# Kernel optimization log

Measured on AMD Instinct MI355X. Metric: run time of the kernel, lower is better.

Reference implementation:

```python
import jax, jax.numpy as jnp
import numpy as np

B, S, H = 1, 1024, 2048
NH, HD = 16, 128
E, K, FI, SFI = 8, 2, 1408, 2816
EPS = 1e-6
THETA = 10000.0


def setup_inputs() -> dict:
    key = jax.random.key(0)
    ks = jax.random.split(key, 14)
    sc = 0.02
    return {
        "hidden_states": jax.random.normal(ks[0], (B, S, H), jnp.float32),
        "ln1_w": jnp.ones((H,), jnp.float32),
        "ln2_w": jnp.ones((H,), jnp.float32),
        "wq": jax.random.normal(ks[1], (H, H), jnp.float32) * sc,
        "wk": jax.random.normal(ks[2], (H, H), jnp.float32) * sc,
        "wv": jax.random.normal(ks[3], (H, H), jnp.float32) * sc,
        "wo": jax.random.normal(ks[4], (H, H), jnp.float32) * sc,
        "gate_w": jax.random.normal(ks[5], (E, H), jnp.float32) * sc,
        "expert_gate": jax.random.normal(ks[6], (E, FI, H), jnp.float32) * sc,
        "expert_up": jax.random.normal(ks[7], (E, FI, H), jnp.float32) * sc,
        "expert_down": jax.random.normal(ks[8], (E, H, FI), jnp.float32) * sc,
        "shared_gate": jax.random.normal(ks[9], (SFI, H), jnp.float32) * sc,
        "shared_up": jax.random.normal(ks[10], (SFI, H), jnp.float32) * sc,
        "shared_down": jax.random.normal(ks[11], (H, SFI), jnp.float32) * sc,
    }


def _rmsnorm(x, w):
    v = jnp.mean(x * x, axis=-1, keepdims=True)
    return x * jax.lax.rsqrt(v + EPS) * w


def _rotate_half(x):
    x1, x2 = x[..., : HD // 2], x[..., HD // 2 :]
    return jnp.concatenate((-x2, x1), axis=-1)


def _rope_cos_sin():
    inv_freq = 1.0 / (THETA ** (jnp.arange(0, HD, 2, dtype=jnp.float32) / HD))
    t = jnp.arange(S, dtype=jnp.float32)
    freqs = t[:, None] * inv_freq[None, :]          # [S, HD//2]
    emb = jnp.concatenate((freqs, freqs), axis=-1)  # [S, HD]
    return jnp.cos(emb)[None, None], jnp.sin(emb)[None, None]  # [1,1,S,HD]


def _decoder_layer(hidden_states, ln1_w, ln2_w, wq, wk, wv, wo, gate_w,
                   expert_gate, expert_up, expert_down,
                   shared_gate, shared_up, shared_down):
    # ---- self-attention ----
    residual = hidden_states
    h = _rmsnorm(hidden_states, ln1_w)
    q = (h @ wq.T).reshape(B, S, NH, HD).transpose(0, 2, 1, 3)  # [B,NH,S,HD]
    k = (h @ wk.T).reshape(B, S, NH, HD).transpose(0, 2, 1, 3)
    v = (h @ wv.T).reshape(B, S, NH, HD).transpose(0, 2, 1, 3)
    cos, sin = _rope_cos_sin()
    q = q * cos + _rotate_half(q) * sin
    k = k * cos + _rotate_half(k) * sin
    scores = jnp.einsum('bhqd,bhkd->bhqk', q, k) / jnp.sqrt(jnp.float32(HD))
    causal = jnp.tril(jnp.ones((S, S), bool))
    scores = jnp.where(causal[None, None], scores, jnp.finfo(jnp.float32).min)
    probs = jax.nn.softmax(scores, axis=-1)
    attn = jnp.einsum('bhqk,bhkd->bhqd', probs, v)
    attn = attn.transpose(0, 2, 1, 3).reshape(B, S, H)
    x = residual + attn @ wo.T

    # ---- MoE MLP ----
    residual = x
    h2 = _rmsnorm(x, ln2_w)
    flat = h2.reshape(-1, H)                       # [N,H], N=B*S
    n_tok = flat.shape[0]
    logits = flat @ gate_w.T                       # [N,E]
    gate_scores = jax.nn.softmax(logits, axis=-1)
    topk_w, topk_idx = jax.lax.top_k(gate_scores, K)
    topk_w = topk_w / (jnp.sum(topk_w, axis=-1, keepdims=True) + 1e-20)
    # dense combine weights [N,E] (zero for unrouted experts)
    combine = jnp.zeros((n_tok, E), flat.dtype).at[
        jnp.arange(n_tok)[:, None], topk_idx].add(topk_w)
    # SwiGLU per expert, dense over all experts, then weighted combine
    g = jnp.einsum('nh,efh->enf', flat, expert_gate)   # [E,N,FI]
    u = jnp.einsum('nh,efh->enf', flat, expert_up)
    act = jax.nn.silu(g) * u
    eo = jnp.einsum('enf,ehf->enh', act, expert_down)  # [E,N,H]
    routed = jnp.einsum('enh,ne->nh', eo, combine)
    # shared experts (always on)
    shared = (jax.nn.silu(flat @ shared_gate.T) * (flat @ shared_up.T)) @ shared_down.T
    return residual + (routed + shared).reshape(B, S, H)


def reference(hidden_states, ln1_w, ln2_w, wq, wk, wv, wo, gate_w,
              expert_gate, expert_up, expert_down,
              shared_gate, shared_up, shared_down):
    return _decoder_layer(hidden_states, ln1_w, ln2_w, wq, wk, wv, wo, gate_w,
                          expert_gate, expert_up, expert_down,
                          shared_gate, shared_up, shared_down)
```

## Files before the change

kernel.cpp:

```cpp
#include <hip/hip_runtime.h>
#include <hip/hip_bf16.h>


#define DI __device__ __forceinline__

typedef __attribute__((ext_vector_type(8))) short short8;
typedef __attribute__((ext_vector_type(4))) float f32x4;
using u16 = unsigned short;

struct alignas(8) U16x4 { u16 x, y, z, w; };

DI u16 f2bf(float f) {
  unsigned u = __float_as_uint(f);
  u += 0x7fffu + ((u >> 16) & 1u);
  return (u16)(u >> 16);
}
DI float bf2f(u16 h) { return __uint_as_float(((unsigned)h) << 16); }

DI void gload16(const void* g, void* l) {
  __builtin_amdgcn_global_load_lds((const __attribute__((address_space(1))) void*)g,
                                   (__attribute__((address_space(3))) void*)l, 16, 0, 0);
}


__global__ __launch_bounds__(256) void k_ropetab(float* __restrict__ tab) {
  int idx = blockIdx.x * 256 + threadIdx.x;
  int s = idx >> 6, i = idx & 63;
  double inv = pow(10000.0, -(double)(2 * i) / 128.0);
  double ang = (double)s * inv;
  tab[idx * 2 + 0] = (float)cos(ang);
  tab[idx * 2 + 1] = (float)sin(ang);
}

__global__ __launch_bounds__(256) void k_rmsnorm(const float* __restrict__ in,
                                                 const float* __restrict__ w,
                                                 float* __restrict__ outf,
                                                 u16* __restrict__ outh,
                                                 u16* __restrict__ outl) {
  const int row = blockIdx.x, t = threadIdx.x;
  const float* x = in + (size_t)row * 2048;
  float4 a = *(const float4*)&x[t * 4];
  float4 b = *(const float4*)&x[1024 + t * 4];
  float ss = a.x * a.x + a.y * a.y + a.z * a.z + a.w * a.w +
             b.x * b.x + b.y * b.y + b.z * b.z + b.w * b.w;
#pragma unroll
  for (int off = 32; off; off >>= 1) ss += __shfl_xor(ss, off);
  __shared__ float red[4];
  if ((t & 63) == 0) red[t >> 6] = ss;
  __syncthreads();
  float total = red[0] + red[1] + red[2] + red[3];
  float r = 1.0f / sqrtf(total * (1.0f / 2048.0f) + 1e-6f);
  float4 wa = *(const float4*)&w[t * 4];
  float4 wb = *(const float4*)&w[1024 + t * 4];
  float va[8] = {a.x * r * wa.x, a.y * r * wa.y, a.z * r * wa.z, a.w * r * wa.w,
                 b.x * r * wb.x, b.y * r * wb.y, b.z * r * wb.z, b.w * r * wb.w};
  if (outf) {
    *(float4*)&outf[(size_t)row * 2048 + t * 4] = make_float4(va[0], va[1], va[2], va[3]);
    *(float4*)&outf[(size_t)row * 2048 + 1024 + t * 4] = make_float4(va[4], va[5], va[6], va[7]);
  }
  if (outh) {
    U16x4 ha{f2bf(va[0]), f2bf(va[1]), f2bf(va[2]), f2bf(va[3])};
    U16x4 hb{f2bf(va[4]), f2bf(va[5]), f2bf(va[6]), f2bf(va[7])};
    *(U16x4*)&outh[(size_t)row * 2048 + t * 4] = ha;
    *(U16x4*)&outh[(size_t)row * 2048 + 1024 + t * 4] = hb;
    if (outl) {
      U16x4 la{f2bf(va[0] - bf2f(ha.x)), f2bf(va[1] - bf2f(ha.y)),
               f2bf(va[2] - bf2f(ha.z)), f2bf(va[3] - bf2f(ha.w))};
      U16x4 lb{f2bf(va[4] - bf2f(hb.x)), f2bf(va[5] - bf2f(hb.y)),
               f2bf(va[6] - bf2f(hb.z)), f2bf(va[7] - bf2f(hb.w))};
      *(U16x4*)&outl[(size_t)row * 2048 + t * 4] = la;
      *(U16x4*)&outl[(size_t)row * 2048 + 1024 + t * 4] = lb;
    }
  }
}

__global__ __launch_bounds__(256) void k_splitf(const float* __restrict__ src,
                                                u16* __restrict__ dh,
                                                u16* __restrict__ dl) {
  int idx = (blockIdx.x * 256 + threadIdx.x) * 4;
  float4 v = *(const float4*)&src[idx];
  U16x4 h{f2bf(v.x), f2bf(v.y), f2bf(v.z), f2bf(v.w)};
  U16x4 l{f2bf(v.x - bf2f(h.x)), f2bf(v.y - bf2f(h.y)),
          f2bf(v.z - bf2f(h.z)), f2bf(v.w - bf2f(h.w))};
  *(U16x4*)&dh[idx] = h;
  *(U16x4*)&dl[idx] = l;
}

__global__ __launch_bounds__(256) void k_rope(float* __restrict__ q, float* __restrict__ k,
                                              const float* __restrict__ tab) {
  int idx = blockIdx.x * 256 + threadIdx.x;
  int s = idx >> 10, rem = idx & 1023;
  int h = rem >> 6, i = rem & 63;
  size_t base = (size_t)s * 2048 + h * 128 + i;
  float c = tab[(s * 64 + i) * 2 + 0];
  float sn = tab[(s * 64 + i) * 2 + 1];
  const float qs = 0.08838834764831845f;
  float q1 = q[base], q2 = q[base + 64];
  q[base] = (q1 * c - q2 * sn) * qs;
  q[base + 64] = (q2 * c + q1 * sn) * qs;
  float k1 = k[base], k2 = k[base + 64];
  k[base] = k1 * c - k2 * sn;
  k[base + 64] = k2 * c + k1 * sn;
}

__global__ __launch_bounds__(256) void k_splitkv(
    const float* __restrict__ qf, const float* __restrict__ kf,
    const float* __restrict__ vf,
    u16* __restrict__ Qh, u16* __restrict__ Ql,
    u16* __restrict__ Kh, u16* __restrict__ Kl,
    u16* __restrict__ Vth, u16* __restrict__ Vtl) {
  int idx = (blockIdx.x * 256 + threadIdx.x) * 4;
  int s = idx >> 11, c = idx & 2047;
  float4 q4 = *(const float4*)&qf[idx];
  U16x4 qh{f2bf(q4.x), f2bf(q4.y), f2bf(q4.z), f2bf(q4.w)};
  U16x4 ql{f2bf(q4.x - bf2f(qh.x)), f2bf(q4.y - bf2f(qh.y)),
           f2bf(q4.z - bf2f(qh.z)), f2bf(q4.w - bf2f(qh.w))};
  *(U16x4*)&Qh[idx] = qh; *(U16x4*)&Ql[idx] = ql;
  float4 k4 = *(const float4*)&kf[idx];
  U16x4 kh{f2bf(k4.x), f2bf(k4.y), f2bf(k4.z), f2bf(k4.w)};
  U16x4 kl{f2bf(k4.x - bf2f(kh.x)), f2bf(k4.y - bf2f(kh.y)),
           f2bf(k4.z - bf2f(kh.z)), f2bf(k4.w - bf2f(kh.w))};
  *(U16x4*)&Kh[idx] = kh; *(U16x4*)&Kl[idx] = kl;
  float4 v4 = *(const float4*)&vf[idx];
  float vv[4] = {v4.x, v4.y, v4.z, v4.w};
#pragma unroll
  for (int i = 0; i < 4; ++i) {
    u16 hv = f2bf(vv[i]);
    u16 lv = f2bf(vv[i] - bf2f(hv));
    Vth[(size_t)(c + i) * 1024 + s] = hv;
    Vtl[(size_t)(c + i) * 1024 + s] = lv;
  }
}

DI void stage_kv(const u16* __restrict__ Khg, const u16* __restrict__ Klg,
                 const u16* __restrict__ Vhg, const u16* __restrict__ Vlg,
                 u16* lsKh, u16* lsKl, u16* lsVh, u16* lsVl,
                 int kvb, int hh, int wv, int lane) {
#pragma unroll
  for (int it = 0; it < 4; ++it) {
    const int ebase = it * 2048 + wv * 512;
    const int eo = ebase + lane * 8;
    {
      const int rr = eo >> 7, cg = (eo >> 3) & 15;
      const size_t src = (size_t)(kvb + rr) * 2048 + hh * 128 + ((cg ^ (rr & 7)) << 3);
      gload16(Khg + src, lsKh + ebase);
      gload16(Klg + src, lsKl + ebase);
    }
    {
      const int rr = eo >> 6, cg = (eo >> 3) & 7;
      const size_t src = (size_t)(hh * 128 + rr) * 1024 + kvb + ((cg ^ (rr & 7)) << 3);
      gload16(Vhg + src, lsVh + ebase);
      gload16(Vlg + src, lsVl + ebase);
    }
  }
}

__global__ __launch_bounds__(256) void k_attn_tile(
    const u16* __restrict__ Qh, const u16* __restrict__ Ql,
    const u16* __restrict__ Khg, const u16* __restrict__ Klg,
    const u16* __restrict__ Vhg, const u16* __restrict__ Vlg,
    u16* __restrict__ atth, u16* __restrict__ attl) {
  __shared__ u16 lsKh[2][8192], lsKl[2][8192], lsVh[2][8192], lsVl[2][8192];
  __shared__ u16 Plh[4][16][72], Pll[4][16][72];
  const int hh = blockIdx.y;
  const int qb = blockIdx.x * 64;
  const int tid = threadIdx.x, lane = tid & 63, wv = tid >> 6;
  const int l15 = lane & 15, grp = lane >> 4;
  u16(*plh)[72] = Plh[wv];
  u16(*pll)[72] = Pll[wv];
  const int q_glob = qb + wv * 16 + l15;
  const int tend = blockIdx.x + 1;

  short8 qfh[4], qfl[4];
  const size_t qbase = (size_t)q_glob * 2048 + hh * 128;
#pragma unroll
  for (int c = 0; c < 4; ++c) {
    qfh[c] = *(const short8*)&Qh[qbase + c * 32 + grp * 8];
    qfl[c] = *(const short8*)&Ql[qbase + c * 32 + grp * 8];
  }
  f32x4 oacc[8];
#pragma unroll
  for (int dc = 0; dc < 8; ++dc) oacc[dc] = 0.f;
  float m_run = -1e30f, l_run = 0.f;

  int cur = 0;
  stage_kv(Khg, Klg, Vhg, Vlg, lsKh[0], lsKl[0], lsVh[0], lsVl[0], 0, hh, wv, lane);
  __syncthreads();

  for (int kt = 0; kt < tend; ++kt) {
    const int kvb = kt * 64;
    if (kt + 1 < tend)
      stage_kv(Khg, Klg, Vhg, Vlg, lsKh[cur ^ 1], lsKl[cur ^ 1], lsVh[cur ^ 1],
               lsVl[cur ^ 1], kvb + 64, hh, wv, lane);
    const u16* kh = lsKh[cur];
    const u16* kl = lsKl[cur];
    const u16* vh = lsVh[cur];
    const u16* vl = lsVl[cur];

    f32x4 s4[4];
#pragma unroll
    for (int sub = 0; sub < 4; ++sub) {
      f32x4 a = {0.f, 0.f, 0.f, 0.f};
      const int kr = sub * 16 + l15;
      const int sw = kr & 7;
#pragma unroll
      for (int c = 0; c < 4; ++c) {
        const int off = kr * 128 + ((((c << 2) | grp) ^ sw) << 3);
        short8 khf = *(const short8*)&kh[off];
        short8 klf = *(const short8*)&kl[off];
        a = __builtin_amdgcn_mfma_f32_16x16x32_bf16(khf, qfh[c], a, 0, 0, 0);
        a = __builtin_amdgcn_mfma_f32_16x16x32_bf16(klf, qfh[c], a, 0, 0, 0);
        a = __builtin_amdgcn_mfma_f32_16x16x32_bf16(khf, qfl[c], a, 0, 0, 0);
      }
      s4[sub] = a;
    }
    if (kt == tend - 1) {
#pragma unroll
      for (int sub = 0; sub < 4; ++sub)
#pragma unroll
        for (int r = 0; r < 4; ++r) {
          int kv = kvb + sub * 16 + grp * 4 + r;
          if (kv > q_glob) s4[sub][r] = -1e30f;
        }
    }
    float tmax = s4[0][0];
#pragma unroll
    for (int sub = 0; sub < 4; ++sub)
#pragma unroll
      for (int r = 0; r < 4; ++r) tmax = fmaxf(tmax, s4[sub][r]);
    tmax = fmaxf(tmax, __shfl_xor(tmax, 16));
    tmax = fmaxf(tmax, __shfl_xor(tmax, 32));
    float mnew = fmaxf(m_run, tmax);
    float scale = expf(m_run - mnew);
    float p[16], lsum = 0.f;
#pragma unroll
    for (int sub = 0; sub < 4; ++sub)
#pragma unroll
      for (int r = 0; r < 4; ++r) {
        float pe = expf(s4[sub][r] - mnew);
        p[sub * 4 + r] = pe;
        lsum += pe;
      }
    lsum += __shfl_xor(lsum, 16);
    lsum += __shfl_xor(lsum, 32);
    l_run = l_run * scale + lsum;
    m_run = mnew;
#pragma unroll
    for (int dc = 0; dc < 8; ++dc) oacc[dc] *= scale;
#pragma unroll
    for (int sub = 0; sub < 4; ++sub)
#pragma unroll
      for (int rp = 0; rp < 2; ++rp) {
        int i0 = sub * 4 + rp * 2;
        u16 h0 = f2bf(p[i0]), h1 = f2bf(p[i0 + 1]);
        u16 lo0 = f2bf(p[i0] - bf2f(h0)), lo1 = f2bf(p[i0 + 1] - bf2f(h1));
        int kvoff = sub * 16 + grp * 4 + rp * 2;
        *(unsigned*)&plh[l15][kvoff] = (unsigned)h0 | ((unsigned)h1 << 16);
        *(unsigned*)&pll[l15][kvoff] = (unsigned)lo0 | ((unsigned)lo1 << 16);
      }
    short8 phf[2], plf[2];
#pragma unroll
    for (int ks = 0; ks < 2; ++ks) {
      phf[ks] = *(const short8*)&plh[l15][ks * 32 + grp * 8];
      plf[ks] = *(const short8*)&pll[l15][ks * 32 + grp * 8];
    }
#pragma unroll
    for (int dc = 0; dc < 8; ++dc) {
      const int dr = dc * 16 + l15;
      const int sw = dr & 7;
      f32x4 acc = oacc[dc];
#pragma unroll
      for (int ks = 0; ks < 2; ++ks) {
        const int voff = dr * 64 + ((((ks << 2) | grp) ^ sw) << 3);
        short8 vhf = *(const short8*)&vh[voff];
        short8 vlf = *(const short8*)&vl[voff];
        acc = __builtin_amdgcn_mfma_f32_16x16x32_bf16(vhf, phf[ks], acc, 0, 0, 0);
        acc = __builtin_amdgcn_mfma_f32_16x16x32_bf16(vlf, phf[ks], acc, 0, 0, 0);
        acc = __builtin_amdgcn_mfma_f32_16x16x32_bf16(vhf, plf[ks], acc, 0, 0, 0);
      }
      oacc[dc] = acc;
    }
    __syncthreads();
    cur ^= 1;
  }
  float inv = 1.0f / l_run;
#pragma unroll
  for (int dc = 0; dc < 8; ++dc)
#pragma unroll
    for (int rp = 0; rp < 2; ++rp) {
      float v0 = oacc[dc][rp * 2] * inv;
      float v1 = oacc[dc][rp * 2 + 1] * inv;
      u16 h0 = f2bf(v0), h1 = f2bf(v1);
      u16 lo0 = f2bf(v0 - bf2f(h0)), lo1 = f2bf(v1 - bf2f(h1));
      size_t o = (size_t)q_glob * 2048 + hh * 128 + dc * 16 + grp * 4 + rp * 2;
      *(unsigned*)&atth[o] = (unsigned)h0 | ((unsigned)h1 << 16);
      *(unsigned*)&attl[o] = (unsigned)lo0 | ((unsigned)lo1 << 16);
    }
}

__global__ __launch_bounds__(256) void k_router(const float* __restrict__ h2f,
                                                const float* __restrict__ gw,
                                                int2* __restrict__ tidx,
                                                float2* __restrict__ twgt) {
  const int tok = blockIdx.x;
  const float* hrow = h2f + (size_t)tok * 2048;
  float part[8];
#pragma unroll
  for (int e = 0; e < 8; ++e) part[e] = 0.f;
  for (int j = 0; j < 8; ++j) {
    int p = j * 256 + threadIdx.x;
    float hv = hrow[p];
#pragma unroll
    for (int e = 0; e < 8; ++e) part[e] += hv * gw[e * 2048 + p];
  }
#pragma unroll
  for (int e = 0; e < 8; ++e)
#pragma unroll
    for (int off = 32; off; off >>= 1) part[e] += __shfl_xor(part[e], off);
  __shared__ float red[4][8];
  int wv = threadIdx.x >> 6, lane = threadIdx.x & 63;
  if (lane == 0) {
#pragma unroll
    for (int e = 0; e < 8; ++e) red[wv][e] = part[e];
  }
  __syncthreads();
  if (threadIdx.x == 0) {
    float lg[8];
#pragma unroll
    for (int e = 0; e < 8; ++e) lg[e] = red[0][e] + red[1][e] + red[2][e] + red[3][e];
    float m = lg[0];
#pragma unroll
    for (int e = 1; e < 8; ++e) m = fmaxf(m, lg[e]);
    float ex[8], s = 0.f;
#pragma unroll
    for (int e = 0; e < 8; ++e) { ex[e] = expf(lg[e] - m); s += ex[e]; }
#pragma unroll
    for (int e = 0; e < 8; ++e) ex[e] /= s;
    int i1 = 0;
#pragma unroll
    for (int e = 1; e < 8; ++e) if (ex[e] > ex[i1]) i1 = e;
    int i2 = (i1 == 0) ? 1 : 0;
#pragma unroll
    for (int e = 0; e < 8; ++e) if (e != i1 && ex[e] > ex[i2]) i2 = e;
    float s2 = ex[i1] + ex[i2] + 1e-20f;
    tidx[tok] = make_int2(i1, i2);
    twgt[tok] = make_float2(ex[i1] / s2, ex[i2] / s2);
  }
}

__global__ __launch_bounds__(64) void k_scan(const int2* __restrict__ tidx,
                                             const float2* __restrict__ twgt,
                                             int* __restrict__ meta,
                                             int* __restrict__ toklist,
                                             float* __restrict__ slotw,
                                             int* __restrict__ slots) {
  const int lane = threadIdx.x;
  int base = 0;
  for (int e = 0; e < 8; ++e) {
    int cnt = 0;
    for (int c = 0; c < 16; ++c) {
      const int tok = c * 64 + lane;
      int2 my = tidx[tok];
      int f1 = (my.x == e), f2 = (my.y == e);
      int flag = f1 | f2;
      unsigned long long m = __ballot(flag);
      if (flag) {
        float2 w = twgt[tok];
        int rank = (int)__popcll(m & ((1ull << lane) - 1ull));
        int s = base + cnt + rank;
        toklist[s] = tok;
        slotw[s] = f1 ? w.x : w.y;
        slots[tok * 2 + (f1 ? 0 : 1)] = s;
      }
      cnt += (int)__popcll(m);
    }
    if (lane == 0) { meta[e] = base; meta[9 + e] = cnt; }
    const int padded = ((cnt + 127) >> 7) << 7;
    for (int s = cnt + lane; s < padded; s += 64) {
      toklist[base + s] = 0;
      slotw[base + s] = 0.f;
    }
    base += padded;
  }
  if (lane == 0) meta[8] = base;
}


DI void stageA_bf16(const u16* __restrict__ A, size_t lda, int row0, int k0,
                    u16* lsA, int tid) {
  const int lane = tid & 63, wv = tid >> 6;
#pragma unroll
  for (int it = 0; it < 2; ++it) {
    const int ebase = it * 2048 + wv * 512;
    const int eo = ebase + lane * 8;
    const int rr = eo >> 5, cc = eo & 31;
    gload16(A + (size_t)(row0 + rr) * lda + k0 + cc, lsA + ebase);
  }
}
DI void stageB_f32(const float* __restrict__ B, size_t ldb, int row0, int k0,
                   u16* lsB, int tid) {
#pragma unroll
  for (int j = 0; j < 4; ++j) {
    const int eo = (j * 256 + tid) * 4;
    const int rr = eo >> 5, cc = eo & 31;
    float4 bv = *(const float4*)(B + (size_t)(row0 + rr) * ldb + k0 + cc);
    U16x4 hv{f2bf(bv.x), f2bf(bv.y), f2bf(bv.z), f2bf(bv.w)};
    *(U16x4*)&lsB[eo] = hv;
  }
}
DI void stageB64_f32(const float* __restrict__ B, size_t ldb, int row0, int k0,
                     u16* lsB, int tid) {
#pragma unroll
  for (int j = 0; j < 2; ++j) {
    const int eo = (j * 256 + tid) * 4;
    const int rr = eo >> 5, cc = eo & 31;
    float4 bv = *(const float4*)(B + (size_t)(row0 + rr) * ldb + k0 + cc);
    U16x4 hv{f2bf(bv.x), f2bf(bv.y), f2bf(bv.z), f2bf(bv.w)};
    *(U16x4*)&lsB[eo] = hv;
  }
}

__global__ __launch_bounds__(256) void k_gemm_bf16split(
    const u16* __restrict__ Ah, const u16* __restrict__ Al,
    const u16* __restrict__ Bh0, const u16* __restrict__ Bl0,
    const u16* __restrict__ Bh1, const u16* __restrict__ Bl1,
    const u16* __restrict__ Bh2, const u16* __restrict__ Bl2,
    float* __restrict__ C0, float* __restrict__ C1, float* __restrict__ C2,
    const float* __restrict__ resid) {
  __shared__ u16 lsAh[4096], lsAl[4096], lsBh[4096], lsBl[4096];
  const int z = blockIdx.z;
  const u16* Bh = (z == 0) ? Bh0 : (z == 1) ? Bh1 : Bh2;
  const u16* Bl = (z == 0) ? Bl0 : (z == 1) ? Bl1 : Bl2;
  float* Cm = (z == 0) ? C0 : (z == 1) ? C1 : C2;
  const int tid = threadIdx.x, lane = tid & 63, wv = tid >> 6;
  const int wr = (wv >> 1) * 64, wc = (wv & 1) * 64;
  const int fr = lane & 15, fg = lane >> 4;
  const int row0 = blockIdx.x * 128, col0 = blockIdx.y * 128;
  f32x4 acc[4][4];
#pragma unroll
  for (int i = 0; i < 4; ++i)
#pragma unroll
    for (int j = 0; j < 4; ++j) acc[i][j] = 0.f;

  for (int kt = 0; kt < 64; ++kt) {
    const int k0 = kt * 32;
    stageA_bf16(Ah, 2048, row0, k0, lsAh, tid);
    stageA_bf16(Al, 2048, row0, k0, lsAl, tid);
    stageA_bf16(Bh, 2048, col0, k0, lsBh, tid);
    stageA_bf16(Bl, 2048, col0, k0, lsBl, tid);
    __syncthreads();
    short8 ah[4], al[4], bh[4], bl[4];
#pragma unroll
    for (int mi = 0; mi < 4; ++mi) {
      const int off = (wr + mi * 16 + fr) * 32 + fg * 8;
      ah[mi] = *(const short8*)&lsAh[off];
      al[mi] = *(const short8*)&lsAl[off];
    }
#pragma unroll
    for (int ni = 0; ni < 4; ++ni) {
      const int off = (wc + ni * 16 + fr) * 32 + fg * 8;
      bh[ni] = *(const short8*)&lsBh[off];
      bl[ni] = *(const short8*)&lsBl[off];
    }
#pragma unroll
    for (int mi = 0; mi < 4; ++mi)
#pragma unroll
      for (int ni = 0; ni < 4; ++ni) {
        f32x4 c = acc[mi][ni];
        c = __builtin_amdgcn_mfma_f32_16x16x32_bf16(al[mi], bh[ni], c, 0, 0, 0);
        c = __builtin_amdgcn_mfma_f32_16x16x32_bf16(ah[mi], bl[ni], c, 0, 0, 0);
        c = __builtin_amdgcn_mfma_f32_16x16x32_bf16(ah[mi], bh[ni], c, 0, 0, 0);
        acc[mi][ni] = c;
      }
    __syncthreads();
  }
  const bool hasres = (resid != nullptr);
#pragma unroll
  for (int mi = 0; mi < 4; ++mi)
#pragma unroll
    for (int ni = 0; ni < 4; ++ni)
#pragma unroll
      for (int qq = 0; qq < 4; ++qq) {
        const int row = row0 + wr + mi * 16 + fg * 4 + qq;
        const int col = col0 + wc + ni * 16 + fr;
        float val = acc[mi][ni][qq];
        if (hasres) val += resid[(size_t)row * 2048 + col];
        Cm[(size_t)row * 2048 + col] = val;
      }
}

DI int tile_to_expert(const int* meta, int t) {
  int e = 0;
  while (e < 7 && t >= (meta[e + 1] >> 7)) ++e;
  return e;
}

__global__ __launch_bounds__(256) void k_dual_all(
    const u16* __restrict__ h2b, const float* __restrict__ eg,
    const float* __restrict__ eu, const float* __restrict__ sg,
    const float* __restrict__ su, const int* __restrict__ meta,
    const int* __restrict__ toklist, const float* __restrict__ slotw,
    u16* __restrict__ act, u16* __restrict__ acts) {
  const int bid = blockIdx.x;
  const bool isShared = bid >= 528;
  __shared__ int toks[128];
  __shared__ u16 lsA[4096], lsG[2048], lsU[2048];
  const int tid = threadIdx.x, lane = tid & 63, wv = tid >> 6;
  const int wr = (wv >> 1) * 64, wc = (wv & 1) * 32;
  const int fr = lane & 15, fg = lane >> 4;

  int n0, e = 0, off_e = 0, cnt_e = 0, rtile = 0;
  const float *Bg, *Bu;
  if (isShared) {
    const int b2 = bid - 528;
    rtile = b2 / 44;
    n0 = (b2 % 44) * 64;
    Bg = sg;
    Bu = su;
    if (tid < 128) toks[tid] = rtile * 128 + tid;
  } else {
    const int t = bid / 22;
    if (t >= (meta[8] >> 7)) return;
    n0 = (bid % 22) * 64;
    e = tile_to_expert(meta, t);
    off_e = meta[e];
    cnt_e = meta[9 + e];
    rtile = t - (off_e >> 7);
    Bg = eg + (size_t)e * 1408 * 2048;
    Bu = eu + (size_t)e * 1408 * 2048;
    if (tid < 128) toks[tid] = toklist[off_e + rtile * 128 + tid] & 1023;
  }
  f32x4 ag[4][2], au[4][2];
#pragma unroll
  for (int i = 0; i < 4; ++i)
#pragma unroll
    for (int j = 0; j < 2; ++j) { ag[i][j] = 0.f; au[i][j] = 0.f; }
  __syncthreads();

  for (int kt = 0; kt < 64; ++kt) {
    const int k0 = kt * 32;
#pragma unroll
    for (int it = 0; it < 2; ++it) {
      const int ebase = it * 2048 + wv * 512;
      const int eo = ebase + lane * 8;
      const int rr = eo >> 5, cc = eo & 31;
      gload16(h2b + (size_t)toks[rr] * 2048 + k0 + cc, lsA + ebase);
    }
#pragma unroll
    for (int j = 0; j < 2; ++j) {
      const int eo = (j * 256 + tid) * 4;
      const int rr = eo >> 5, cc = eo & 31;
      float4 gv = *(const float4*)(Bg + (size_t)(n0 + rr) * 2048 + k0 + cc);
      float4 uv = *(const float4*)(Bu + (size_t)(n0 + rr) * 2048 + k0 + cc);
      U16x4 gh{f2bf(gv.x), f2bf(gv.y), f2bf(gv.z), f2bf(gv.w)};
      U16x4 uh{f2bf(uv.x), f2bf(uv.y), f2bf(uv.z), f2bf(uv.w)};
      *(U16x4*)&lsG[eo] = gh;
      *(U16x4*)&lsU[eo] = uh;
    }
    __syncthreads();
    short8 af[4], gf[2], uf[2];
#pragma unroll
    for (int mi = 0; mi < 4; ++mi)
      af[mi] = *(const short8*)&lsA[(wr + mi * 16 + fr) * 32 + fg * 8];
#pragma unroll
    for (int ni = 0; ni < 2; ++ni) {
      const int off = (wc + ni * 16 + fr) * 32 + fg * 8;
      gf[ni] = *(const short8*)&lsG[off];
      uf[ni] = *(const short8*)&lsU[off];
    }
#pragma unroll
    for (int mi = 0; mi < 4; ++mi)
#pragma unroll
      for (int ni = 0; ni < 2; ++ni) {
        ag[mi][ni] = __builtin_amdgcn_mfma_f32_16x16x32_bf16(af[mi], gf[ni], ag[mi][ni], 0, 0, 0);
        au[mi][ni] = __builtin_amdgcn_mfma_f32_16x16x32_bf16(af[mi], uf[ni], au[mi][ni], 0, 0, 0);
      }
    __syncthreads();
  }
#pragma unroll
  for (int mi = 0; mi < 4; ++mi)
#pragma unroll
    for (int ni = 0; ni < 2; ++ni)
#pragma unroll
      for (int qq = 0; qq < 4; ++qq) {
        const int r = wr + mi * 16 + fg * 4 + qq;
        const int col = n0 + wc + ni * 16 + fr;
        float g = ag[mi][ni][qq], u = au[mi][ni][qq];
        float a = g / (1.0f + expf(-g)) * u;
        if (isShared) {
          acts[(size_t)(rtile * 128 + r) * 2816 + col] = f2bf(a);
        } else {
          const int rowInE = rtile * 128 + r;
          if (rowInE < cnt_e)
            act[(size_t)(off_e + rowInE) * 1408 + col] = f2bf(a * slotw[off_e + rowInE]);
        }
      }
}

__global__ __launch_bounds__(256) void k_down_all(
    const u16* __restrict__ act, const float* __restrict__ ed,
    const u16* __restrict__ acts, const float* __restrict__ sd,
    const int* __restrict__ meta, float* __restrict__ dwn,
    float* __restrict__ shd) {
  __shared__ u16 lsA[4096], lsB[4096];
  const int bid = blockIdx.x;
  const int tid = threadIdx.x, lane = tid & 63, wv = tid >> 6;
  const int fr = lane & 15, fg = lane >> 4;
  if (bid < 384) {
    const int t = bid >> 4;
    if (t >= (meta[8] >> 7)) return;
    const int col0 = (bid & 15) * 128;
    const int e = tile_to_expert(meta, t);
    const int off_e = meta[e];
    const int rtile = t - (off_e >> 7);
    const int wr = (wv >> 1) * 64, wc = (wv & 1) * 64;
    const u16* Ab = act + (size_t)off_e * 1408;
    const float* Bb = ed + (size_t)e * 2048 * 1408;
    f32x4 acc[4][4];
#pragma unroll
    for (int i = 0; i < 4; ++i)
#pragma unroll
      for (int j = 0; j < 4; ++j) acc[i][j] = 0.f;
    for (int kt = 0; kt < 44; ++kt) {
      const int k0 = kt * 32;
      stageA_bf16(Ab, 1408, rtile * 128, k0, lsA, tid);
      stageB_f32(Bb, 1408, col0, k0, lsB, tid);
      __syncthreads();
      short8 af[4], bf_[4];
#pragma unroll
      for (int mi = 0; mi < 4; ++mi)
        af[mi] = *(const short8*)&lsA[(wr + mi * 16 + fr) * 32 + fg * 8];
#pragma unroll
      for (int ni = 0; ni < 4; ++ni)
        bf_[ni] = *(const short8*)&lsB[(wc + ni * 16 + fr) * 32 + fg * 8];
#pragma unroll
      for (int mi = 0; mi < 4; ++mi)
#pragma unroll
        for (int ni = 0; ni < 4; ++ni)
          acc[mi][ni] = __builtin_amdgcn_mfma_f32_16x16x32_bf16(af[mi], bf_[ni], acc[mi][ni], 0, 0, 0);
      __syncthreads();
    }
#pragma unroll
    for (int mi = 0; mi < 4; ++mi)
#pragma unroll
      for (int ni = 0; ni < 4; ++ni)
#pragma unroll
        for (int qq = 0; qq < 4; ++qq) {
          const int r = wr + mi * 16 + fg * 4 + qq;
          const int col = col0 + wc + ni * 16 + fr;
          dwn[(size_t)(off_e + rtile * 128 + r) * 2048 + col] = acc[mi][ni][qq];
        }
  } else {
    const int b2 = bid - 384;
    const int row0 = (b2 >> 5) * 128;
    const int col0 = (b2 & 31) * 64;
    const int wr = (wv >> 1) * 64, wc = (wv & 1) * 32;
    f32x4 acc[4][2];
#pragma unroll
    for (int i = 0; i < 4; ++i)
#pragma unroll
      for (int j = 0; j < 2; ++j) acc[i][j] = 0.f;
    for (int kt = 0; kt < 88; ++kt) {
      const int k0 = kt * 32;
      stageA_bf16(acts, 2816, row0, k0, lsA, tid);
      stageB64_f32(sd, 2816, col0, k0, lsB, tid);
      __syncthreads();
      short8 af[4], bf_[2];
#pragma unroll
      for (int mi = 0; mi < 4; ++mi)
        af[mi] = *(const short8*)&lsA[(wr + mi * 16 + fr) * 32 + fg * 8];
#pragma unroll
      for (int ni = 0; ni < 2; ++ni)
        bf_[ni] = *(const short8*)&lsB[(wc + ni * 16 + fr) * 32 + fg * 8];
#pragma unroll
      for (int mi = 0; mi < 4; ++mi)
#pragma unroll
        for (int ni = 0; ni < 2; ++ni)
          acc[mi][ni] = __builtin_amdgcn_mfma_f32_16x16x32_bf16(af[mi], bf_[ni], acc[mi][ni], 0, 0, 0);
      __syncthreads();
    }
#pragma unroll
    for (int mi = 0; mi < 4; ++mi)
#pragma unroll
      for (int ni = 0; ni < 2; ++ni)
#pragma unroll
        for (int qq = 0; qq < 4; ++qq) {
          const int row = row0 + wr + mi * 16 + fg * 4 + qq;
          const int col = col0 + wc + ni * 16 + fr;
          shd[(size_t)row * 2048 + col] = acc[mi][ni][qq];
        }
  }
}

__global__ __launch_bounds__(256) void k_combine(
    const float* __restrict__ shd, const float* __restrict__ x,
    const float* __restrict__ dwn, const int* __restrict__ slots,
    float* __restrict__ outp) {
  const int i4 = (blockIdx.x * 256 + threadIdx.x) * 4;
  const int row = i4 >> 11, col = i4 & 2047;
  const int s0 = slots[row * 2], s1 = slots[row * 2 + 1];
  float4 a = *(const float4*)&shd[i4];
  float4 b = *(const float4*)&x[i4];
  float4 c = *(const float4*)&dwn[(size_t)s0 * 2048 + col];
  float4 d = *(const float4*)&dwn[(size_t)s1 * 2048 + col];
  float4 o;
  o.x = a.x + b.x + c.x + d.x;
  o.y = a.y + b.y + c.y + d.y;
  o.z = a.z + b.z + c.z + d.z;
  o.w = a.w + b.w + c.w + d.w;
  *(float4*)&outp[i4] = o;
}


extern "C" void kernel_launch(void* const* d_in, const int* in_sizes, int n_in,
                              void* d_out, int out_size, void* d_ws, size_t ws_size,
                              hipStream_t stream) {
  (void)in_sizes; (void)n_in; (void)out_size; (void)ws_size;
  const float* hidden = (const float*)d_in[0];
  const float* ln1 = (const float*)d_in[1];
  const float* ln2 = (const float*)d_in[2];
  const float* wq = (const float*)d_in[3];
  const float* wk = (const float*)d_in[4];
  const float* wvw = (const float*)d_in[5];
  const float* wo = (const float*)d_in[6];
  const float* gw = (const float*)d_in[7];
  const float* eg = (const float*)d_in[8];
  const float* eu = (const float*)d_in[9];
  const float* ed = (const float*)d_in[10];
  const float* sg = (const float*)d_in[11];
  const float* su = (const float*)d_in[12];
  const float* sd = (const float*)d_in[13];
  float* out = (float*)d_out;
  char* ws = (char*)d_ws;

  const size_t KB = 1ull << 10, MB = 1ull << 20;
  float* tab = (float*)(ws + 0);
  int2* tidx = (int2*)(ws + 512 * KB);
  float2* twgt = (float2*)(ws + 520 * KB);
  int* meta = (int*)(ws + 528 * KB);
  int* tokl = (int*)(ws + 532 * KB);
  float* slw = (float*)(ws + 544 * KB);
  int* slots = (int*)(ws + 556 * KB);
  u16* hnh = (u16*)(ws + 1 * MB);
  u16* hnl = (u16*)(ws + 5 * MB);
  u16* wqh = (u16*)(ws + 9 * MB);
  u16* wql = (u16*)(ws + 17 * MB);
  u16* wkh = (u16*)(ws + 25 * MB);
  u16* wkl = (u16*)(ws + 33 * MB);
  u16* wvh = (u16*)(ws + 41 * MB);
  u16* wvl = (u16*)(ws + 49 * MB);
  u16* woh = (u16*)(ws + 57 * MB);
  u16* wol = (u16*)(ws + 65 * MB);
  float* qf = (float*)(ws + 73 * MB);
  float* kf = (float*)(ws + 81 * MB);
  float* vf = (float*)(ws + 89 * MB);
  u16* Qh = (u16*)(ws + 9 * MB);
  u16* Ql = (u16*)(ws + 13 * MB);
  u16* Kh = (u16*)(ws + 17 * MB);
  u16* Kl = (u16*)(ws + 21 * MB);
  u16* Vth = (u16*)(ws + 25 * MB);
  u16* Vtl = (u16*)(ws + 29 * MB);
  u16* atth = (u16*)(ws + 33 * MB);
  u16* attl = (u16*)(ws + 37 * MB);
  float* xf = (float*)(ws + 41 * MB);
  float* h2f = (float*)(ws + 49 * MB);
  u16* h2b = (u16*)(ws + 1 * MB);
  u16* act = (u16*)(ws + 73 * MB);
  u16* acts = (u16*)(ws + 82 * MB);
  float* dwn = (float*)(ws + 9 * MB);
  float* shd = (float*)(ws + 33 * MB);

  k_ropetab<<<256, 256, 0, stream>>>(tab);
  k_rmsnorm<<<1024, 256, 0, stream>>>(hidden, ln1, nullptr, hnh, hnl);
  k_splitf<<<4096, 256, 0, stream>>>(wq, wqh, wql);
  k_splitf<<<4096, 256, 0, stream>>>(wk, wkh, wkl);
  k_splitf<<<4096, 256, 0, stream>>>(wvw, wvh, wvl);
  k_splitf<<<4096, 256, 0, stream>>>(wo, woh, wol);
  k_gemm_bf16split<<<dim3(8, 16, 3), 256, 0, stream>>>(
      hnh, hnl, wqh, wql, wkh, wkl, wvh, wvl, qf, kf, vf, nullptr);
  k_rope<<<4096, 256, 0, stream>>>(qf, kf, tab);
  k_splitkv<<<2048, 256, 0, stream>>>(qf, kf, vf, Qh, Ql, Kh, Kl, Vth, Vtl);
  k_attn_tile<<<dim3(16, 16), 256, 0, stream>>>(Qh, Ql, Kh, Kl, Vth, Vtl, atth, attl);
  k_gemm_bf16split<<<dim3(8, 16, 1), 256, 0, stream>>>(
      atth, attl, woh, wol, woh, wol, woh, wol, xf, xf, xf, hidden);
  k_rmsnorm<<<1024, 256, 0, stream>>>(xf, ln2, h2f, h2b, nullptr);
  k_router<<<1024, 256, 0, stream>>>(h2f, gw, tidx, twgt);
  k_scan<<<1, 64, 0, stream>>>(tidx, twgt, meta, tokl, slw, slots);
  k_dual_all<<<880, 256, 0, stream>>>(h2b, eg, eu, sg, su, meta, tokl, slw, act, acts);
  k_down_all<<<640, 256, 0, stream>>>(act, ed, acts, sd, meta, dwn, shd);
  k_combine<<<2048, 256, 0, stream>>>(shd, xf, dwn, slots, out);
}
```

Before: 609.0 us.

## Double-buffer LDS tiles and prefetch next K-slice in MoE expert GEMMs

Converts the gate/up and down-projection expert GEMM loops to a two-stage software pipeline. The next K tile's activations are issued via global_load_lds into the alternate LDS buffer, and the fp32 weights are held in registers while the current tile's MFMAs run. The weights are converted to bf16 and written to LDS after the MFMAs, which hides global-load latency and drops one barrier per iteration. In exchange it doubles LDS use and raises register pressure, which may reduce occupancy.

```diff
diff --git a/kernel.cpp b/kernel.cpp
--- a/kernel.cpp
+++ b/kernel.cpp
@@ -397,25 +397,22 @@
     gload16(A + (size_t)(row0 + rr) * lda + k0 + cc, lsA + ebase);
   }
 }
-DI void stageB_f32(const float* __restrict__ B, size_t ldb, int row0, int k0,
-                   u16* lsB, int tid) {
-#pragma unroll
-  for (int j = 0; j < 4; ++j) {
+template <int NJ>
+DI void loadB_regs(const float* __restrict__ B, size_t ldb, int row0, int k0,
+                   int tid, float4* r) {
+#pragma unroll
+  for (int j = 0; j < NJ; ++j) {
     const int eo = (j * 256 + tid) * 4;
     const int rr = eo >> 5, cc = eo & 31;
-    float4 bv = *(const float4*)(B + (size_t)(row0 + rr) * ldb + k0 + cc);
-    U16x4 hv{f2bf(bv.x), f2bf(bv.y), f2bf(bv.z), f2bf(bv.w)};
-    *(U16x4*)&lsB[eo] = hv;
-  }
-}
-DI void stageB64_f32(const float* __restrict__ B, size_t ldb, int row0, int k0,
-                     u16* lsB, int tid) {
-#pragma unroll
-  for (int j = 0; j < 2; ++j) {
+    r[j] = *(const float4*)(B + (size_t)(row0 + rr) * ldb + k0 + cc);
+  }
+}
+template <int NJ>
+DI void writeB_lds(u16* lsB, int tid, const float4* r) {
+#pragma unroll
+  for (int j = 0; j < NJ; ++j) {
     const int eo = (j * 256 + tid) * 4;
-    const int rr = eo >> 5, cc = eo & 31;
-    float4 bv = *(const float4*)(B + (size_t)(row0 + rr) * ldb + k0 + cc);
-    U16x4 hv{f2bf(bv.x), f2bf(bv.y), f2bf(bv.z), f2bf(bv.w)};
+    U16x4 hv{f2bf(r[j].x), f2bf(r[j].y), f2bf(r[j].z), f2bf(r[j].w)};
     *(U16x4*)&lsB[eo] = hv;
   }
 }
@@ -504,7 +501,7 @@
   const int bid = blockIdx.x;
   const bool isShared = bid >= 528;
   __shared__ int toks[128];
-  __shared__ u16 lsA[4096], lsG[2048], lsU[2048];
+  __shared__ u16 lsA[2][4096], lsG[2][2048], lsU[2][2048];
   const int tid = threadIdx.x, lane = tid & 63, wv = tid >> 6;
   const int wr = (wv >> 1) * 64, wc = (wv & 1) * 32;
   const int fr = lane & 15, fg = lane >> 4;
@@ -537,36 +534,42 @@
     for (int j = 0; j < 2; ++j) { ag[i][j] = 0.f; au[i][j] = 0.f; }
   __syncthreads();
 
-  for (int kt = 0; kt < 64; ++kt) {
-    const int k0 = kt * 32;
+  auto stageAg = [&](u16* dst, int k0) {
 #pragma unroll
     for (int it = 0; it < 2; ++it) {
       const int ebase = it * 2048 + wv * 512;
       const int eo = ebase + lane * 8;
       const int rr = eo >> 5, cc = eo & 31;
-      gload16(h2b + (size_t)toks[rr] * 2048 + k0 + cc, lsA + ebase);
-    }
-#pragma unroll
-    for (int j = 0; j < 2; ++j) {
-      const int eo = (j * 256 + tid) * 4;
-      const int rr = eo >> 5, cc = eo & 31;
-      float4 gv = *(const float4*)(Bg + (size_t)(n0 + rr) * 2048 + k0 + cc);
-      float4 uv = *(const float4*)(Bu + (size_t)(n0 + rr) * 2048 + k0 + cc);
-      U16x4 gh{f2bf(gv.x), f2bf(gv.y), f2bf(gv.z), f2bf(gv.w)};
-      U16x4 uh{f2bf(uv.x), f2bf(uv.y), f2bf(uv.z), f2bf(uv.w)};
-      *(U16x4*)&lsG[eo] = gh;
-      *(U16x4*)&lsU[eo] = uh;
-    }
-    __syncthreads();
+      gload16(h2b + (size_t)toks[rr] * 2048 + k0 + cc, dst + ebase);
+    }
+  };
+
+  float4 gpre[2], upre[2];
+  stageAg(lsA[0], 0);
+  loadB_regs<2>(Bg, 2048, n0, 0, tid, gpre);
+  loadB_regs<2>(Bu, 2048, n0, 0, tid, upre);
+  writeB_lds<2>(lsG[0], tid, gpre);
+  writeB_lds<2>(lsU[0], tid, upre);
+  __syncthreads();
+
+  int cur = 0;
+  for (int kt = 0; kt < 64; ++kt) {
+    const int k1 = (kt + 1) * 32;
+    const bool pf = (kt + 1 < 64);
+    if (pf) {
+      stageAg(lsA[cur ^ 1], k1);
+      loadB_regs<2>(Bg, 2048, n0, k1, tid, gpre);
+      loadB_regs<2>(Bu, 2048, n0, k1, tid, upre);
+    }
     short8 af[4], gf[2], uf[2];
 #pragma unroll
     for (int mi = 0; mi < 4; ++mi)
-      af[mi] = *(const short8*)&lsA[(wr + mi * 16 + fr) * 32 + fg * 8];
+      af[mi] = *(const short8*)&lsA[cur][(wr + mi * 16 + fr) * 32 + fg * 8];
 #pragma unroll
     for (int ni = 0; ni < 2; ++ni) {
       const int off = (wc + ni * 16 + fr) * 32 + fg * 8;
-      gf[ni] = *(const short8*)&lsG[off];
-      uf[ni] = *(const short8*)&lsU[off];
+      gf[ni] = *(const short8*)&lsG[cur][off];
+      uf[ni] = *(const short8*)&lsU[cur][off];
     }
 #pragma unroll
     for (int mi = 0; mi < 4; ++mi)
@@ -575,7 +578,12 @@
         ag[mi][ni] = __builtin_amdgcn_mfma_f32_16x16x32_bf16(af[mi], gf[ni], ag[mi][ni], 0, 0, 0);
         au[mi][ni] = __builtin_amdgcn_mfma_f32_16x16x32_bf16(af[mi], uf[ni], au[mi][ni], 0, 0, 0);
       }
+    if (pf) {
+      writeB_lds<2>(lsG[cur ^ 1], tid, gpre);
+      writeB_lds<2>(lsU[cur ^ 1], tid, upre);
+    }
     __syncthreads();
+    cur ^= 1;
   }
 #pragma unroll
   for (int mi = 0; mi < 4; ++mi)
@@ -602,7 +610,7 @@
     const u16* __restrict__ acts, const float* __restrict__ sd,
     const int* __restrict__ meta, float* __restrict__ dwn,
     float* __restrict__ shd) {
-  __shared__ u16 lsA[4096], lsB[4096];
+  __shared__ u16 lsA[2][4096], lsB[2][4096];
   const int bid = blockIdx.x;
   const int tid = threadIdx.x, lane = tid & 63, wv = tid >> 6;
   const int fr = lane & 15, fg = lane >> 4;
@@ -621,24 +629,34 @@
     for (int i = 0; i < 4; ++i)
 #pragma unroll
       for (int j = 0; j < 4; ++j) acc[i][j] = 0.f;
+    float4 bpre[4];
+    stageA_bf16(Ab, 1408, rtile * 128, 0, lsA[0], tid);
+    loadB_regs<4>(Bb, 1408, col0, 0, tid, bpre);
+    writeB_lds<4>(lsB[0], tid, bpre);
+    __syncthreads();
+    int cur = 0;
     for (int kt = 0; kt < 44; ++kt) {
-      const int k0 = kt * 32;
-      stageA_bf16(Ab, 1408, rtile * 128, k0, lsA, tid);
-      stageB_f32(Bb, 1408, col0, k0, lsB, tid);
-      __syncthreads();
+      const int k1 = (kt + 1) * 32;
+      const bool pf = (kt + 1 < 44);
+      if (pf) {
+        stageA_bf16(Ab, 1408, rtile * 128, k1, lsA[cur ^ 1], tid);
+        loadB_regs<4>(Bb, 1408, col0, k1, tid, bpre);
+      }
       short8 af[4], bf_[4];
 #pragma unroll
       for (int mi = 0; mi < 4; ++mi)
-        af[mi] = *(const short8*)&lsA[(wr + mi * 16 + fr) * 32 + fg * 8];
+        af[mi] = *(const short8*)&lsA[cur][(wr + mi * 16 + fr) * 32 + fg * 8];
 #pragma unroll
       for (int ni = 0; ni < 4; ++ni)
-        bf_[ni] = *(const short8*)&lsB[(wc + ni * 16 + fr) * 32 + fg * 8];
+        bf_[ni] = *(const short8*)&lsB[cur][(wc + ni * 16 + fr) * 32 + fg * 8];
 #pragma unroll
       for (int mi = 0; mi < 4; ++mi)
 #pragma unroll
         for (int ni = 0; ni < 4; ++ni)
           acc[mi][ni] = __builtin_amdgcn_mfma_f32_16x16x32_bf16(af[mi], bf_[ni], acc[mi][ni], 0, 0, 0);
+      if (pf) writeB_lds<4>(lsB[cur ^ 1], tid, bpre);
       __syncthreads();
+      cur ^= 1;
     }
 #pragma unroll
     for (int mi = 0; mi < 4; ++mi)
@@ -660,24 +678,34 @@
     for (int i = 0; i < 4; ++i)
 #pragma unroll
       for (int j = 0; j < 2; ++j) acc[i][j] = 0.f;
+    float4 bpre[2];
+    stageA_bf16(acts, 2816, row0, 0, lsA[0], tid);
+    loadB_regs<2>(sd, 2816, col0, 0, tid, bpre);
+    writeB_lds<2>(lsB[0], tid, bpre);
+    __syncthreads();
+    int cur = 0;
     for (int kt = 0; kt < 88; ++kt) {
-      const int k0 = kt * 32;
-      stageA_bf16(acts, 2816, row0, k0, lsA, tid);
-      stageB64_f32(sd, 2816, col0, k0, lsB, tid);
-      __syncthreads();
+      const int k1 = (kt + 1) * 32;
+      const bool pf = (kt + 1 < 88);
+      if (pf) {
+        stageA_bf16(acts, 2816, row0, k1, lsA[cur ^ 1], tid);
+        loadB_regs<2>(sd, 2816, col0, k1, tid, bpre);
+      }
       short8 af[4], bf_[2];
 #pragma unroll
       for (int mi = 0; mi < 4; ++mi)
-        af[mi] = *(const short8*)&lsA[(wr + mi * 16 + fr) * 32 + fg * 8];
+        af[mi] = *(const short8*)&lsA[cur][(wr + mi * 16 + fr) * 32 + fg * 8];
 #pragma unroll
       for (int ni = 0; ni < 2; ++ni)
-        bf_[ni] = *(const short8*)&lsB[(wc + ni * 16 + fr) * 32 + fg * 8];
+        bf_[ni] = *(const short8*)&lsB[cur][(wc + ni * 16 + fr) * 32 + fg * 8];
 #pragma unroll
       for (int mi = 0; mi < 4; ++mi)
 #pragma unroll
         for (int ni = 0; ni < 2; ++ni)
           acc[mi][ni] = __builtin_amdgcn_mfma_f32_16x16x32_bf16(af[mi], bf_[ni], acc[mi][ni], 0, 0, 0);
+      if (pf) writeB_lds<2>(lsB[cur ^ 1], tid, bpre);
       __syncthreads();
+      cur ^= 1;
     }
 #pragma unroll
     for (int mi = 0; mi < 4; ++mi)
```

After: 590.1 us. 3.1% less time.
